# Kernel optimization log

Measured on AMD Instinct MI355X. Metric: run time of the kernel, lower is better.

Reference implementation:

```python
import jax, jax.numpy as jnp
import numpy as np
from jax import lax

B, DIM, H, W = 16, 512, 56, 56
STYLE, LAT, K, PADW = 64, 8, 7, 3
HID = 4 * DIM
EPS = 1e-6


def setup_inputs() -> dict:
    key = jax.random.key(0)
    ks = jax.random.split(key, 12)
    f = lambda k, shp: jax.random.normal(k, shp, dtype=jnp.float32)
    sc = 0.02  # small init so per-sample generated weights are well-scaled
    d = {}
    d['x'] = f(ks[0], (B, DIM, H, W))
    d['s'] = f(ks[1], (B, STYLE))
    # depthwise hyperconv: style -> latent -> kernel [DIM, 1, K, K]
    d['dw_fc_w'] = f(ks[2], (STYLE, LAT)) * sc
    d['dw_fc_b'] = jnp.zeros((LAT,), jnp.float32)
    d['dw_param'] = f(ks[3], (LAT, DIM, 1, K, K)) * sc
    d['dw_bfc_w'] = f(ks[4], (STYLE, DIM)) * sc
    d['dw_bfc_b'] = jnp.zeros((DIM,), jnp.float32)
    # channels-first LayerNorm affine
    d['ln_w'] = jnp.ones((DIM,), jnp.float32)
    d['ln_b'] = jnp.zeros((DIM,), jnp.float32)
    # pointwise hyperconv 1: DIM -> 4*DIM (1x1)
    d['pw1_fc_w'] = f(ks[5], (STYLE, LAT)) * sc
    d['pw1_fc_b'] = jnp.zeros((LAT,), jnp.float32)
    d['pw1_param'] = f(ks[6], (LAT, HID, DIM)) * sc
    d['pw1_bfc_w'] = f(ks[7], (STYLE, HID)) * sc
    d['pw1_bfc_b'] = jnp.zeros((HID,), jnp.float32)
    # pointwise hyperconv 2: 4*DIM -> DIM (1x1)
    d['pw2_fc_w'] = f(ks[8], (STYLE, LAT)) * sc
    d['pw2_fc_b'] = jnp.zeros((LAT,), jnp.float32)
    d['pw2_param'] = f(ks[9], (LAT, DIM, HID)) * sc
    d['pw2_bfc_w'] = f(ks[10], (STYLE, DIM)) * sc
    d['pw2_bfc_b'] = jnp.zeros((DIM,), jnp.float32)
    # layer scale gamma, init 1e-6
    d['gamma'] = jnp.full((1, DIM, 1, 1), 1e-6, jnp.float32)
    return d


def _forward(x, s, dw_fc_w, dw_fc_b, dw_param, dw_bfc_w, dw_bfc_b,
             ln_w, ln_b,
             pw1_fc_w, pw1_fc_b, pw1_param, pw1_bfc_w, pw1_bfc_b,
             pw2_fc_w, pw2_fc_b, pw2_param, pw2_bfc_w, pw2_bfc_b,
             gamma):
    xin = x
    # reflection pad (ReflectionPad2d(PADW))
    xp = jnp.pad(x, ((0, 0), (0, 0), (PADW, PADW), (PADW, PADW)), mode='reflect')

    # --- depthwise hyperconv: per-sample generated 7x7 depthwise kernel ---
    z_dw = s @ dw_fc_w + dw_fc_b                                   # [B, LAT]
    w_dw = jnp.einsum('bl,lcikj->bcikj', z_dw, dw_param)           # [B, DIM, 1, K, K]
    b_dw = s @ dw_bfc_w + dw_bfc_b                                 # [B, DIM]

    def dwconv_one(xi, wi):
        # xi: [DIM, Hp, Wp]; wi: [DIM, 1, K, K]; depthwise (groups=DIM), VALID
        return lax.conv_general_dilated(xi[None], wi, (1, 1), 'VALID',
                                        feature_group_count=DIM)[0]
    x = jax.vmap(dwconv_one)(xp, w_dw) + b_dw[:, :, None, None]    # [B, DIM, H, W]

    # --- channels-first LayerNorm (biased variance over channel dim) ---
    u = x.mean(1, keepdims=True)
    v = jnp.square(x - u).mean(1, keepdims=True)
    x = (x - u) * lax.rsqrt(v + EPS)
    x = ln_w[None, :, None, None] * x + ln_b[None, :, None, None]

    # --- pointwise hyperconv 1 (1x1): DIM -> 4*DIM, per-sample weight ---
    z1 = s @ pw1_fc_w + pw1_fc_b
    w1 = jnp.einsum('bl,loi->boi', z1, pw1_param)                  # [B, HID, DIM]
    b1 = s @ pw1_bfc_w + pw1_bfc_b                                 # [B, HID]
    x = jnp.einsum('boi,bihw->bohw', w1, x) + b1[:, :, None, None]

    # exact GELU (torch nn.GELU default)
    x = jax.nn.gelu(x, approximate=False)

    # --- pointwise hyperconv 2 (1x1): 4*DIM -> DIM, per-sample weight ---
    z2 = s @ pw2_fc_w + pw2_fc_b
    w2 = jnp.einsum('bl,loi->boi', z2, pw2_param)                  # [B, DIM, HID]
    b2 = s @ pw2_bfc_w + pw2_bfc_b                                 # [B, DIM]
    x = jnp.einsum('boi,bihw->bohw', w2, x) + b2[:, :, None, None]

    x = gamma * x
    return xin + x


def reference(x, s, dw_fc_w, dw_fc_b, dw_param, dw_bfc_w, dw_bfc_b,
              ln_w, ln_b,
              pw1_fc_w, pw1_fc_b, pw1_param, pw1_bfc_w, pw1_bfc_b,
              pw2_fc_w, pw2_fc_b, pw2_param, pw2_bfc_w, pw2_bfc_b,
              gamma):
    return _forward(x, s, dw_fc_w, dw_fc_b, dw_param, dw_bfc_w, dw_bfc_b,
                    ln_w, ln_b,
                    pw1_fc_w, pw1_fc_b, pw1_param, pw1_bfc_w, pw1_bfc_b,
                    pw2_fc_w, pw2_fc_b, pw2_param, pw2_bfc_w, pw2_bfc_b,
                    gamma)
```

## Files before the change

### kernel.cpp

```cpp
#include <hip/hip_runtime.h>

#define NB    16
#define DIM   512
#define HH    56
#define WW    56
#define HWPIX 3136
#define HID   2048
#define NSTYLE 64
#define NLAT   8

typedef float f32x4 __attribute__((ext_vector_type(4)));
typedef __bf16 bf16x8 __attribute__((ext_vector_type(8)));
typedef unsigned short u16x8 __attribute__((ext_vector_type(8)));

__device__ __forceinline__ unsigned short f2bf(float f) {
  unsigned u = __float_as_uint(f);
  u += 0x7fffu + ((u >> 16) & 1u);
  return (unsigned short)(u >> 16);
}

__device__ __forceinline__ void gload16(const void* g, void* l) {
  __builtin_amdgcn_global_load_lds((__attribute__((address_space(1))) void*)g,
                                   (__attribute__((address_space(3))) void*)l,
                                   16, 0, 0);
}

__global__ __launch_bounds__(256)
void k_small(const float* __restrict__ s,
             const float* __restrict__ dw_fc_w, const float* __restrict__ dw_fc_b,
             const float* __restrict__ dw_bfc_w, const float* __restrict__ dw_bfc_b,
             const float* __restrict__ p1_fc_w, const float* __restrict__ p1_fc_b,
             const float* __restrict__ p1_bfc_w, const float* __restrict__ p1_bfc_b,
             const float* __restrict__ p2_fc_w, const float* __restrict__ p2_fc_b,
             const float* __restrict__ p2_bfc_w, const float* __restrict__ p2_bfc_b,
             float* __restrict__ z_dw, float* __restrict__ z1, float* __restrict__ z2,
             float* __restrict__ b_dw, float* __restrict__ b1, float* __restrict__ b2) {
  int b = blockIdx.x, t = threadIdx.x;
  __shared__ float ls[NSTYLE];
  if (t < NSTYLE) ls[t] = s[b*NSTYLE + t];
  __syncthreads();
  if (t < NLAT) {
    float a0 = dw_fc_b[t], a1 = p1_fc_b[t], a2 = p2_fc_b[t];
    for (int j = 0; j < NSTYLE; ++j) {
      float sv = ls[j];
      a0 += sv * dw_fc_w[j*NLAT + t];
      a1 += sv * p1_fc_w[j*NLAT + t];
      a2 += sv * p2_fc_w[j*NLAT + t];
    }
    z_dw[b*NLAT + t] = a0; z1[b*NLAT + t] = a1; z2[b*NLAT + t] = a2;
  }
  for (int c = t; c < DIM; c += 256) {
    float a = dw_bfc_b[c], a2 = p2_bfc_b[c];
    for (int j = 0; j < NSTYLE; ++j) {
      float sv = ls[j];
      a  += sv * dw_bfc_w[j*DIM + c];
      a2 += sv * p2_bfc_w[j*DIM + c];
    }
    b_dw[b*DIM + c] = a; b2[b*DIM + c] = a2;
  }
  for (int c = t; c < HID; c += 256) {
    float a = p1_bfc_b[c];
    for (int j = 0; j < NSTYLE; ++j) a += ls[j] * p1_bfc_w[j*HID + c];
    b1[b*HID + c] = a;
  }
}

__global__ __launch_bounds__(256)
void k_wdw(const float* __restrict__ z_dw, const float* __restrict__ dw_param,
           float* __restrict__ wdw) {
  int idx = blockIdx.x * 256 + threadIdx.x;
  if (idx >= NB*DIM) return;
  int b = idx >> 9, c = idx & 511;
  float z[NLAT];
#pragma unroll
  for (int ll = 0; ll < NLAT; ++ll) z[ll] = z_dw[b*NLAT + ll];
  for (int k = 0; k < 49; ++k) {
    float a = 0.f;
#pragma unroll
    for (int ll = 0; ll < NLAT; ++ll) a += z[ll] * dw_param[((long)ll*DIM + c)*49 + k];
    wdw[(long)idx*49 + k] = a;
  }
}

__global__ __launch_bounds__(256)
void k_wgen(const float* __restrict__ z, const float* __restrict__ param,
            unsigned short* __restrict__ out, long OI) {
  __shared__ float lz[NB*NLAT];
  if (threadIdx.x < NB*NLAT) lz[threadIdx.x] = z[threadIdx.x];
  __syncthreads();
  long e4 = ((long)blockIdx.x * 256 + threadIdx.x) * 4;
  if (e4 >= OI) return;
  float a[NB][4] = {};
#pragma unroll
  for (int ll = 0; ll < NLAT; ++ll) {
    float4 v = *(const float4*)(param + (long)ll*OI + e4);
#pragma unroll
    for (int b = 0; b < NB; ++b) {
      float zz = lz[b*NLAT + ll];
      a[b][0] += zz*v.x; a[b][1] += zz*v.y; a[b][2] += zz*v.z; a[b][3] += zz*v.w;
    }
  }
#pragma unroll
  for (int b = 0; b < NB; ++b) {
    ushort4 pk;
    pk.x = f2bf(a[b][0]); pk.y = f2bf(a[b][1]); pk.z = f2bf(a[b][2]); pk.w = f2bf(a[b][3]);
    *(ushort4*)(out + (long)b*OI + e4) = pk;
  }
}

__global__ __launch_bounds__(64)
void k_dwconv(const float* __restrict__ x, const float* __restrict__ wdw,
              const float* __restrict__ bdw, float* __restrict__ y) {
  int bc = blockIdx.x;
  const float* xb = x + (long)bc * HWPIX;
  float* yb = y + (long)bc * HWPIX;
  int ox = threadIdx.x;
  bool act = ox < WW;
  int oxc = act ? ox : WW-1;
  int cj[7];
#pragma unroll
  for (int j = 0; j < 7; ++j) {
    int v = oxc + j - 3;
    v = v < 0 ? -v : (v > WW-1 ? 2*(WW-1) - v : v);
    cj[j] = v;
  }
  float wk[49];
#pragma unroll
  for (int k = 0; k < 49; ++k) wk[k] = wdw[(long)bc*49 + k];
  float bias = bdw[bc];
  float acc[7];
#pragma unroll
  for (int j = 0; j < 7; ++j) acc[j] = bias;
#pragma unroll 62
  for (int r = 0; r < HH + 6; ++r) {
    int sy = r - 3;
    sy = sy < 0 ? -sy : (sy > HH-1 ? 2*(HH-1) - sy : sy);
    const float* rowp = xb + sy*WW;
    float v[7];
#pragma unroll
    for (int j = 0; j < 7; ++j) v[j] = rowp[cj[j]];
#pragma unroll
    for (int dy = 0; dy < 7; ++dy) {
      int orow = r - dy;
      if (orow >= 0 && orow < HH) {
        float a = acc[orow % 7];
#pragma unroll
        for (int dx = 0; dx < 7; ++dx) a += v[dx] * wk[dy*7 + dx];
        acc[orow % 7] = a;
      }
    }
    if (r >= 6) {
      int orow = r - 6;
      if (act) yb[orow*WW + oxc] = acc[orow % 7];
      acc[orow % 7] = bias;
    }
  }
}

__global__ __launch_bounds__(256)
void k_ln(const float* __restrict__ y, const float* __restrict__ ln_w,
          const float* __restrict__ ln_b, unsigned short* __restrict__ xln) {
  int b = blockIdx.y;
  int p = blockIdx.x * 256 + threadIdx.x;
  if (p >= HWPIX) return;
  const float* yb = y + (long)b * DIM * HWPIX;
  float s = 0.f, s2 = 0.f;
  for (int c = 0; c < DIM; ++c) {
    float v = yb[(long)c*HWPIX + p];
    s += v; s2 += v*v;
  }
  float mean = s * (1.0f/DIM);
  float var  = s2 * (1.0f/DIM) - mean*mean;
  float rstd = rsqrtf(var + 1e-6f);
  unsigned short* dst = xln + ((long)b*HWPIX + p) * DIM;
  for (int c0 = 0; c0 < DIM; c0 += 8) {
    u16x8 pk;
#pragma unroll
    for (int j = 0; j < 8; ++j) {
      int c = c0 + j;
      float v = (yb[(long)c*HWPIX + p] - mean) * rstd * ln_w[c] + ln_b[c];
      pk[j] = f2bf(v);
    }
    *(u16x8*)(dst + c0) = pk;
  }
}

template<int MODE>
__global__ __launch_bounds__(256)
void k_gemm(const unsigned short* __restrict__ A, const unsigned short* __restrict__ Bt,
            const float* __restrict__ bias,
            unsigned short* __restrict__ hout,
            const float* __restrict__ xin, const float* __restrict__ gamma,
            float* __restrict__ fout,
            int M, int N, int Kd, long sA, long sBt, int sBias) {
  __shared__ unsigned short lsA[128*32];
  __shared__ unsigned short lsB[128*32];
  int bz = blockIdx.z;
  int row0 = blockIdx.y * 128, col0 = blockIdx.x * 128;
  int t = threadIdx.x, l = t & 63, w = t >> 6;
  const unsigned short* Ab  = A  + (long)bz * sA;
  const unsigned short* Btb = Bt + (long)bz * sBt;
  int srow = w*32 + (l >> 2);
  int skb  = (l & 3) * 8;
  const unsigned short* ga = Ab  + (long)(row0 + srow) * Kd + skb;
  const unsigned short* gb = Btb + (long)(col0 + srow) * Kd + skb;
  unsigned short* la = &lsA[srow*32 + skb];
  unsigned short* lb = &lsB[srow*32 + skb];
  int wr = w >> 1, wc = w & 1;
  int rr = l & 15, kg = (l >> 4) * 8;
  f32x4 acc[4][4] = {};
  int nk = Kd >> 5;
  for (int kk = 0; kk < nk; ++kk) {
    gload16(ga, la);
    gload16(ga + 16*(long)Kd, la + 16*32);
    gload16(gb, lb);
    gload16(gb + 16*(long)Kd, lb + 16*32);
    ga += 32; gb += 32;
    __syncthreads();
    bf16x8 af[4], bfr[4];
#pragma unroll
    for (int m = 0; m < 4; ++m)
      af[m] = *(const bf16x8*)&lsA[(wr*64 + m*16 + rr)*32 + kg];
#pragma unroll
    for (int n = 0; n < 4; ++n)
      bfr[n] = *(const bf16x8*)&lsB[(wc*64 + n*16 + rr)*32 + kg];
#pragma unroll
    for (int m = 0; m < 4; ++m)
#pragma unroll
      for (int n = 0; n < 4; ++n)
        acc[m][n] = __builtin_amdgcn_mfma_f32_16x16x32_bf16(af[m], bfr[n], acc[m][n], 0, 0, 0);
    __syncthreads();
  }
  long ob = (long)bz * M * N;
  const float* biasb = bias + (long)bz * sBias;
#pragma unroll
  for (int m = 0; m < 4; ++m) {
#pragma unroll
    for (int n = 0; n < 4; ++n) {
      int col = col0 + wc*64 + n*16 + rr;
#pragma unroll
      for (int j = 0; j < 4; ++j) {
        int row = row0 + wr*64 + m*16 + (l >> 4)*4 + j;
        float v = acc[m][n][j];
        if constexpr (MODE == 1) {
          if (row < M) {
            v += biasb[col];
            v = 0.5f * v * (1.0f + erff(v * 0.70710678118654752f));
            hout[ob + (long)row * N + col] = f2bf(v);
          }
        } else {
          if (col < N) {
            v = (v + biasb[row]) * gamma[row] + xin[ob + (long)row * N + col];
            fout[ob + (long)row * N + col] = v;
          }
        }
      }
    }
  }
}

extern "C" void kernel_launch(void* const* d_in, const int* in_sizes, int n_in,
                              void* d_out, int out_size, void* d_ws, size_t ws_size,
                              hipStream_t stream) {
  (void)in_sizes; (void)n_in; (void)out_size; (void)ws_size;
  const float* x         = (const float*)d_in[0];
  const float* s         = (const float*)d_in[1];
  const float* dw_fc_w   = (const float*)d_in[2];
  const float* dw_fc_b   = (const float*)d_in[3];
  const float* dw_param  = (const float*)d_in[4];
  const float* dw_bfc_w  = (const float*)d_in[5];
  const float* dw_bfc_b  = (const float*)d_in[6];
  const float* ln_w      = (const float*)d_in[7];
  const float* ln_b      = (const float*)d_in[8];
  const float* pw1_fc_w  = (const float*)d_in[9];
  const float* pw1_fc_b  = (const float*)d_in[10];
  const float* pw1_param = (const float*)d_in[11];
  const float* pw1_bfc_w = (const float*)d_in[12];
  const float* pw1_bfc_b = (const float*)d_in[13];
  const float* pw2_fc_w  = (const float*)d_in[14];
  const float* pw2_fc_b  = (const float*)d_in[15];
  const float* pw2_param = (const float*)d_in[16];
  const float* pw2_bfc_w = (const float*)d_in[17];
  const float* pw2_bfc_b = (const float*)d_in[18];
  const float* gamma     = (const float*)d_in[19];
  float* out = (float*)d_out;

  char* ws = (char*)d_ws;
  size_t off = 0;
  auto alloc = [&](size_t bytes) {
    void* p = ws + off;
    off += (bytes + 255) & ~(size_t)255;
    return p;
  };
  float* z_dw = (float*)alloc(NB*NLAT*4);
  float* z1   = (float*)alloc(NB*NLAT*4);
  float* z2   = (float*)alloc(NB*NLAT*4);
  float* b_dw = (float*)alloc((size_t)NB*DIM*4);
  float* b2   = (float*)alloc((size_t)NB*DIM*4);
  float* b1   = (float*)alloc((size_t)NB*HID*4);
  float* wdw  = (float*)alloc((size_t)NB*DIM*49*4);
  unsigned short* w1  = (unsigned short*)alloc((size_t)NB*HID*DIM*2);
  unsigned short* w2  = (unsigned short*)alloc((size_t)NB*DIM*HID*2);
  unsigned short* xln = (unsigned short*)alloc((size_t)NB*HWPIX*DIM*2 + 131072);
  unsigned short* h   = (unsigned short*)alloc((size_t)NB*HWPIX*HID*2 + 524288);

  float* y = out;

  k_small<<<NB, 256, 0, stream>>>(s, dw_fc_w, dw_fc_b, dw_bfc_w, dw_bfc_b,
                                  pw1_fc_w, pw1_fc_b, pw1_bfc_w, pw1_bfc_b,
                                  pw2_fc_w, pw2_fc_b, pw2_bfc_w, pw2_bfc_b,
                                  z_dw, z1, z2, b_dw, b1, b2);
  k_wdw<<<(NB*DIM + 255)/256, 256, 0, stream>>>(z_dw, dw_param, wdw);
  {
    long OI = (long)HID * DIM;
    int blocks = (int)(OI / 4 / 256);
    k_wgen<<<blocks, 256, 0, stream>>>(z1, pw1_param, w1, OI);
    k_wgen<<<blocks, 256, 0, stream>>>(z2, pw2_param, w2, OI);
  }
  k_dwconv<<<NB*DIM, 64, 0, stream>>>(x, wdw, b_dw, y);
  k_ln<<<dim3((HWPIX + 255)/256, NB), 256, 0, stream>>>(y, ln_w, ln_b, xln);

  k_gemm<1><<<dim3(HID/128, (HWPIX + 127)/128, NB), 256, 0, stream>>>(
      xln, w1, b1, h, nullptr, nullptr, nullptr,
      HWPIX, HID, DIM, (long)HWPIX*DIM, (long)HID*DIM, HID);

  k_gemm<2><<<dim3((HWPIX + 127)/128, DIM/128, NB), 256, 0, stream>>>(
      w2, h, b2, nullptr, x, gamma, out,
      DIM, HWPIX, HID, (long)DIM*HID, (long)HWPIX*HID, DIM);
}
```

Before: 1.180 ms.

## Deepen GEMM K-tile with swizzled LDS, rework LayerNorm, use tanh GELU

The GEMM now stages a 64-wide K slice per iteration with an XOR-swizzled LDS layout, which halves the number of barriers and is meant to avoid bank conflicts on fragment reads. LayerNorm is restructured so each block handles 32 pixels with 8 channel groups, reduces the statistics through shared memory, and transposes through LDS so the bf16 writes are coalesced. The exact erf GELU is replaced with the tanh approximation, which changes numerics slightly.

```diff
diff --git a/kernel.cpp b/kernel.cpp
--- a/kernel.cpp
+++ b/kernel.cpp
@@ -23,6 +23,13 @@
   __builtin_amdgcn_global_load_lds((__attribute__((address_space(1))) void*)g,
                                    (__attribute__((address_space(3))) void*)l,
                                    16, 0, 0);
+}
+
+__device__ __forceinline__ float fast_gelu(float x) {
+  float u = 0.7978845608f * x * (1.0f + 0.044715f * x * x);
+  float e = __expf(2.0f * u);
+  float t = 1.0f - 2.0f / (1.0f + e);
+  return 0.5f * x * (1.0f + t);
 }
 
 __global__ __launch_bounds__(256)
@@ -160,28 +167,49 @@
 __global__ __launch_bounds__(256)
 void k_ln(const float* __restrict__ y, const float* __restrict__ ln_w,
           const float* __restrict__ ln_b, unsigned short* __restrict__ xln) {
-  int b = blockIdx.y;
-  int p = blockIdx.x * 256 + threadIdx.x;
-  if (p >= HWPIX) return;
-  const float* yb = y + (long)b * DIM * HWPIX;
+  __shared__ float red[2][8][32];
+  __shared__ float stat[2][32];
+  __shared__ unsigned short T[32][514];
+  int b = blockIdx.y, p0 = blockIdx.x * 32;
+  int t = threadIdx.x, cc = t >> 5, pc = t & 31;
+  const float* yb = y + (long)b * DIM * HWPIX + p0 + pc;
+  float vv[64];
   float s = 0.f, s2 = 0.f;
-  for (int c = 0; c < DIM; ++c) {
-    float v = yb[(long)c*HWPIX + p];
-    s += v; s2 += v*v;
-  }
-  float mean = s * (1.0f/DIM);
-  float var  = s2 * (1.0f/DIM) - mean*mean;
-  float rstd = rsqrtf(var + 1e-6f);
-  unsigned short* dst = xln + ((long)b*HWPIX + p) * DIM;
-  for (int c0 = 0; c0 < DIM; c0 += 8) {
+#pragma unroll
+  for (int j = 0; j < 64; ++j) {
+    float v = yb[(long)(cc*64 + j) * HWPIX];
+    vv[j] = v; s += v; s2 += v*v;
+  }
+  red[0][cc][pc] = s; red[1][cc][pc] = s2;
+  __syncthreads();
+  if (t < 32) {
+    float a = 0.f, a2 = 0.f;
+#pragma unroll
+    for (int k = 0; k < 8; ++k) { a += red[0][k][t]; a2 += red[1][k][t]; }
+    float mean = a * (1.0f/DIM);
+    float var  = a2 * (1.0f/DIM) - mean*mean;
+    stat[0][t] = mean; stat[1][t] = rsqrtf(var + 1e-6f);
+  }
+  __syncthreads();
+  float mean = stat[0][pc], rstd = stat[1][pc];
+#pragma unroll
+  for (int j8 = 0; j8 < 8; ++j8) {
     u16x8 pk;
 #pragma unroll
-    for (int j = 0; j < 8; ++j) {
-      int c = c0 + j;
-      float v = (yb[(long)c*HWPIX + p] - mean) * rstd * ln_w[c] + ln_b[c];
-      pk[j] = f2bf(v);
-    }
-    *(u16x8*)(dst + c0) = pk;
+    for (int jj = 0; jj < 8; ++jj) {
+      int c = cc*64 + j8*8 + jj;
+      pk[jj] = f2bf((vv[j8*8 + jj] - mean) * rstd * ln_w[c] + ln_b[c]);
+    }
+    *(u16x8*)&T[pc][cc*64 + j8*8] = pk;
+  }
+  __syncthreads();
+  unsigned short* dst = xln + ((long)b * HWPIX + p0) * DIM;
+#pragma unroll
+  for (int r = 0; r < 8; ++r) {
+    int idx = r*256 + t;
+    int px = idx >> 6, cl = idx & 63;
+    u16x8 v = *(u16x8*)&T[px][cl*8];
+    *(u16x8*)(dst + (long)px*DIM + cl*8) = v;
   }
 }
 
@@ -193,42 +221,55 @@
             const float* __restrict__ xin, const float* __restrict__ gamma,
             float* __restrict__ fout,
             int M, int N, int Kd, long sA, long sBt, int sBias) {
-  __shared__ unsigned short lsA[128*32];
-  __shared__ unsigned short lsB[128*32];
+  __shared__ unsigned short lsA[128*64];
+  __shared__ unsigned short lsB[128*64];
   int bz = blockIdx.z;
   int row0 = blockIdx.y * 128, col0 = blockIdx.x * 128;
-  int t = threadIdx.x, l = t & 63, w = t >> 6;
+  int t = threadIdx.x, l = t & 63;
   const unsigned short* Ab  = A  + (long)bz * sA;
   const unsigned short* Btb = Bt + (long)bz * sBt;
-  int srow = w*32 + (l >> 2);
-  int skb  = (l & 3) * 8;
-  const unsigned short* ga = Ab  + (long)(row0 + srow) * Kd + skb;
-  const unsigned short* gb = Btb + (long)(col0 + srow) * Kd + skb;
-  unsigned short* la = &lsA[srow*32 + skb];
-  unsigned short* lb = &lsB[srow*32 + skb];
-  int wr = w >> 1, wc = w & 1;
-  int rr = l & 15, kg = (l >> 4) * 8;
+  int rbase = t >> 3;
+  int kcs   = (t & 7) ^ (rbase & 7);
+  const unsigned short* ga = Ab  + (long)(row0 + rbase) * Kd + kcs * 8;
+  const unsigned short* gb = Btb + (long)(col0 + rbase) * Kd + kcs * 8;
+  char* la = (char*)lsA + t * 16;
+  char* lb = (char*)lsB + t * 16;
+  int w = t >> 6, wr = w >> 1, wc = w & 1;
+  int rr = l & 15;
+  int swz = (rr & 7) << 4;
+  int rowA[4], rowB[4];
+#pragma unroll
+  for (int m = 0; m < 4; ++m) rowA[m] = (wr*64 + m*16 + rr) * 128;
+#pragma unroll
+  for (int n = 0; n < 4; ++n) rowB[n] = (wc*64 + n*16 + rr) * 128;
+  int koff[2];
+#pragma unroll
+  for (int ks = 0; ks < 2; ++ks) koff[ks] = ((ks*64 + (l >> 4)*16) ^ swz);
   f32x4 acc[4][4] = {};
-  int nk = Kd >> 5;
+  int nk = Kd >> 6;
+  long r32K = (long)32 * Kd;
   for (int kk = 0; kk < nk; ++kk) {
-    gload16(ga, la);
-    gload16(ga + 16*(long)Kd, la + 16*32);
-    gload16(gb, lb);
-    gload16(gb + 16*(long)Kd, lb + 16*32);
-    ga += 32; gb += 32;
+#pragma unroll
+    for (int j = 0; j < 4; ++j) gload16(ga + j*r32K, la + j*4096);
+#pragma unroll
+    for (int j = 0; j < 4; ++j) gload16(gb + j*r32K, lb + j*4096);
+    ga += 64; gb += 64;
     __syncthreads();
-    bf16x8 af[4], bfr[4];
-#pragma unroll
-    for (int m = 0; m < 4; ++m)
-      af[m] = *(const bf16x8*)&lsA[(wr*64 + m*16 + rr)*32 + kg];
-#pragma unroll
-    for (int n = 0; n < 4; ++n)
-      bfr[n] = *(const bf16x8*)&lsB[(wc*64 + n*16 + rr)*32 + kg];
-#pragma unroll
-    for (int m = 0; m < 4; ++m)
+#pragma unroll
+    for (int ks = 0; ks < 2; ++ks) {
+      bf16x8 af[4], bfr[4];
+#pragma unroll
+      for (int m = 0; m < 4; ++m)
+        af[m] = *(const bf16x8*)((char*)lsA + rowA[m] + koff[ks]);
 #pragma unroll
       for (int n = 0; n < 4; ++n)
-        acc[m][n] = __builtin_amdgcn_mfma_f32_16x16x32_bf16(af[m], bfr[n], acc[m][n], 0, 0, 0);
+        bfr[n] = *(const bf16x8*)((char*)lsB + rowB[n] + koff[ks]);
+#pragma unroll
+      for (int m = 0; m < 4; ++m)
+#pragma unroll
+        for (int n = 0; n < 4; ++n)
+          acc[m][n] = __builtin_amdgcn_mfma_f32_16x16x32_bf16(af[m], bfr[n], acc[m][n], 0, 0, 0);
+    }
     __syncthreads();
   }
   long ob = (long)bz * M * N;
@@ -245,7 +286,7 @@
         if constexpr (MODE == 1) {
           if (row < M) {
             v += biasb[col];
-            v = 0.5f * v * (1.0f + erff(v * 0.70710678118654752f));
+            v = fast_gelu(v);
             hout[ob + (long)row * N + col] = f2bf(v);
           }
         } else {
@@ -318,7 +359,7 @@
     k_wgen<<<blocks, 256, 0, stream>>>(z2, pw2_param, w2, OI);
   }
   k_dwconv<<<NB*DIM, 64, 0, stream>>>(x, wdw, b_dw, y);
-  k_ln<<<dim3((HWPIX + 255)/256, NB), 256, 0, stream>>>(y, ln_w, ln_b, xln);
+  k_ln<<<dim3(HWPIX/32, NB), 256, 0, stream>>>(y, ln_w, ln_b, xln);
 
   k_gemm<1><<<dim3(HID/128, (HWPIX + 127)/128, NB), 256, 0, stream>>>(
       xln, w1, b1, h, nullptr, nullptr, nullptr,
```

Result: faster. 1.116 ms (-5.4%).
